# Kernel tuning notes

Hardware: AMD Instinct MI355X
Metric: run time of the kernel (lower is better)

## Reference

```python
import jax, jax.numpy as jnp
import numpy as np

B, V, P, L, D = 8, 16, 128, 16, 128
PD = L * D  # patch_dim = patch_size * d_model = 2048


def _layernorm(x, g, b, eps=1e-5):
    mu = jnp.mean(x, axis=-1, keepdims=True)
    var = jnp.mean(jnp.square(x - mu), axis=-1, keepdims=True)
    return (x - mu) / jnp.sqrt(var + eps) * g + b


def setup_inputs() -> dict:
    key = jax.random.key(0)
    ks = jax.random.split(key, 24)
    x = jax.random.normal(ks[0], (B, V, P, L, D), jnp.float32)
    m = jax.random.randint(ks[1], (B, V, V), 0, 2) > 0
    var_mask = m & ~jnp.eye(V, dtype=bool)[None]  # keep self-attention unmasked

    def lin_w(k, fan_in, fan_out):
        return jax.random.normal(k, (fan_in, fan_out), jnp.float32) * (1.0 / np.sqrt(fan_in))

    inp = {"x": x, "var_mask": var_mask}
    # Attn_PatchLevel (attn1): query / shared kv / out projections
    inp["w_q1"] = lin_w(ks[2], PD, PD); inp["b_q1"] = jnp.zeros((PD,), jnp.float32)
    inp["w_kv1"] = lin_w(ks[3], PD, PD); inp["b_kv1"] = jnp.zeros((PD,), jnp.float32)
    inp["w_o1"] = lin_w(ks[4], PD, PD); inp["b_o1"] = jnp.zeros((PD,), jnp.float32)
    # Attn_VarLevel (attn2)
    inp["w_q2"] = lin_w(ks[5], PD, PD); inp["b_q2"] = jnp.zeros((PD,), jnp.float32)
    inp["w_kv2"] = lin_w(ks[6], PD, PD); inp["b_kv2"] = jnp.zeros((PD,), jnp.float32)
    inp["w_o2"] = lin_w(ks[7], PD, PD); inp["b_o2"] = jnp.zeros((PD,), jnp.float32)
    # LayerNorms
    inp["g1"] = jnp.ones((PD,), jnp.float32); inp["be1"] = jnp.zeros((PD,), jnp.float32)
    inp["g2"] = jnp.ones((PD,), jnp.float32); inp["be2"] = jnp.zeros((PD,), jnp.float32)
    inp["g3"] = jnp.ones((PD,), jnp.float32); inp["be3"] = jnp.zeros((PD,), jnp.float32)
    # FFN
    inp["w_l1"] = lin_w(ks[8], PD, 4 * PD); inp["b_l1"] = jnp.zeros((4 * PD,), jnp.float32)
    inp["w_l2"] = lin_w(ks[9], 4 * PD, PD); inp["b_l2"] = jnp.zeros((PD,), jnp.float32)
    return inp


def reference(x, var_mask,
              w_q1, b_q1, w_kv1, b_kv1, w_o1, b_o1,
              w_q2, b_q2, w_kv2, b_kv2, w_o2, b_o2,
              g1, be1, g2, be2, g3, be3,
              w_l1, b_l1, w_l2, b_l2):
    b, v, p, l, d = x.shape
    pd = l * d
    scale = 1.0 / np.sqrt(pd)
    x = x.reshape(b, v, p, pd)

    # ---- Attn_PatchLevel (mask=None -> no masking; keys and values share kv_projection) ----
    q = x @ w_q1 + b_q1
    kv = x @ w_kv1 + b_kv1  # keys == values in the original module
    scores = jnp.einsum('bvpd,bvsd->bvps', q, kv)  # [B,V,P,P]
    attn = jax.nn.softmax(scale * scores, axis=-1)  # dropout is identity at eval
    a1 = jnp.einsum('bvps,bvsd->bvpd', attn, kv) @ w_o1 + b_o1
    x = _layernorm(x + a1, g1, be1)

    # ---- Attn_VarLevel over variables, per patch ----
    x = x.transpose(0, 2, 1, 3)  # [B,P,V,PD]
    q = x @ w_q2 + b_q2
    kv = x @ w_kv2 + b_kv2
    scores = jnp.einsum('bpvd,bprd->bpvr', q, kv)  # [B,P,V,V]
    scores = jnp.where(var_mask[:, None, :, :], -jnp.inf, scores)
    attn = jax.nn.softmax(scale * scores, axis=-1)
    a2 = jnp.einsum('bpvr,bprd->bpvd', attn, kv) @ w_o2 + b_o2
    x = _layernorm(x + a2, g2, be2)

    # ---- FFN (torch nn.GELU default = exact erf) ----
    z = jax.nn.gelu(x @ w_l1 + b_l1, approximate=False)
    x = x + z @ w_l2 + b_l2

    x_out = _layernorm(x, g3, be3).transpose(0, 2, 1, 3)  # [B,V,P,PD]
    x_next = x_out.reshape(b, v, p // 2, 2 * l, d)
    return x_out, x_next
```

## Files before the change

kernel.cpp:

```cpp
#include <hip/hip_runtime.h>
#include <math.h>


using u16   = unsigned short;
using f32x4 = __attribute__((ext_vector_type(4))) float;
using bf16x8= __attribute__((ext_vector_type(8))) __bf16;
using u16x8 = __attribute__((ext_vector_type(8))) u16;
using u16x4 = __attribute__((ext_vector_type(4))) u16;

#define NROWS 16384
#define PD    2048
#define MEMBAR asm volatile("" ::: "memory")

__device__ __forceinline__ float bf2f(u16 u) {
    unsigned v = ((unsigned)u) << 16;
    return __builtin_bit_cast(float, v);
}
__device__ __forceinline__ u16 f2bf(float f) {
    unsigned u = __builtin_bit_cast(unsigned, f);
    u += 0x7FFFu + ((u >> 16) & 1u);
    return (u16)(u >> 16);
}
__device__ __forceinline__ void gload_lds16(const void* g, void* l) {
    __builtin_amdgcn_global_load_lds((const __attribute__((address_space(1))) void*)g,
                                     (__attribute__((address_space(3))) void*)l, 16, 0, 0);
}
__device__ __forceinline__ void block_barrier() {
    MEMBAR; __builtin_amdgcn_s_barrier(); MEMBAR;
}

template<int GELU>
__global__ __launch_bounds__(512, 2)
void gemm256(const u16* __restrict__ A, int lda,
             const u16* __restrict__ B, int ldb,
             u16* __restrict__ C1, u16* __restrict__ C2, int ncut, int ldc,
             const float* __restrict__ bias1, const float* __restrict__ bias2,
             int K, int NT, int CM, int CN)
{
    __shared__ __align__(16) char smem[131072];

    const int tid  = threadIdx.x;
    const int wv   = tid >> 6;
    const int wm   = wv >> 2;
    const int wn   = wv & 3;
    const int lane = tid & 63;
    const int fr   = lane & 15;
    const int fks16= (lane >> 4) * 16;
    const int rmask= (fr & 7) << 4;
    const int kb0  = fks16 ^ rmask;
    const int kb1  = (64 + fks16) ^ rmask;

    const int xcd = blockIdx.x & 7;
    const int ii  = blockIdx.x >> 3;
    const int RY  = NT / CN;
    const int mt  = (xcd / RY) * CM + (ii / CN);
    const int nt  = (xcd % RY) * CN + (ii % CN);
    const int m0  = mt * 256;
    const int n0  = nt * 256;

    const int rsub = tid >> 3;
    const int cswE = (((tid & 7) * 16) ^ ((rsub & 7) << 4)) >> 1;
    const int waveByte = wv * 1024;

    auto stage = [&](const u16* mat, int ld, int row0, int k0, int regionByte) {
        const u16* g0 = mat + (size_t)(row0 + rsub) * ld + k0 + cswE;
        gload_lds16(g0,                   smem + regionByte + waveByte);
        gload_lds16(g0 + (size_t)ld * 64, smem + regionByte + 8192 + waveByte);
    };

    const int aRowByte = (wm * 128 + fr) * 128;
    const int bRowByte = (wn * 64 + fr) * 128;

    const int KT = K >> 6;

    stage(A, lda, m0,       0, 0);
    stage(B, ldb, n0,       0, 32768);
    stage(A, lda, m0 + 128, 0, 16384);
    stage(B, ldb, n0 + 128, 0, 49152);
    stage(B, ldb, n0,      64, 98304);
    stage(A, lda, m0,      64, 65536);
    asm volatile("s_waitcnt vmcnt(4)" ::: "memory");
    __builtin_amdgcn_s_barrier();

    bf16x8 a[4][2], b0[2][2], b1[2][2];
    f32x4  acc[8][4] = {};

    for (int t = 0; t < KT; ++t) {
        const int Ab = (t & 1) ? 65536 : 0;
        const int Bb = Ab + 32768;
        const int Ob = Ab ^ 65536;
        const bool s1 = (t + 1 < KT), s2 = (t + 2 < KT);

        #pragma unroll
        for (int mi = 0; mi < 4; ++mi) {
            const int rb = Ab + aRowByte + mi * 2048;
            a[mi][0] = *(const bf16x8*)(smem + rb + kb0);
            a[mi][1] = *(const bf16x8*)(smem + rb + kb1);
        }
        #pragma unroll
        for (int nj = 0; nj < 2; ++nj) {
            const int rb = Bb + bRowByte + nj * 2048;
            b0[nj][0] = *(const bf16x8*)(smem + rb + kb0);
            b0[nj][1] = *(const bf16x8*)(smem + rb + kb1);
        }
        if (s1) stage(B, ldb, n0 + 128, (t + 1) << 6, Ob + 49152);
        __builtin_amdgcn_s_barrier();
        asm volatile("s_waitcnt lgkmcnt(0)" ::: "memory");
        __builtin_amdgcn_sched_barrier(0);
        __builtin_amdgcn_s_setprio(1);
        #pragma unroll
        for (int mi = 0; mi < 4; ++mi)
            #pragma unroll
            for (int nj = 0; nj < 2; ++nj) {
                acc[mi][nj] = __builtin_amdgcn_mfma_f32_16x16x32_bf16(a[mi][0], b0[nj][0], acc[mi][nj], 0, 0, 0);
                acc[mi][nj] = __builtin_amdgcn_mfma_f32_16x16x32_bf16(a[mi][1], b0[nj][1], acc[mi][nj], 0, 0, 0);
            }
        __builtin_amdgcn_s_setprio(0);
        __builtin_amdgcn_s_barrier();

        #pragma unroll
        for (int nj = 0; nj < 2; ++nj) {
            const int rb = Bb + bRowByte + 4096 + nj * 2048;
            b1[nj][0] = *(const bf16x8*)(smem + rb + kb0);
            b1[nj][1] = *(const bf16x8*)(smem + rb + kb1);
        }
        if (s1) stage(A, lda, m0 + 128, (t + 1) << 6, Ob + 16384);
        __builtin_amdgcn_s_barrier();
        asm volatile("s_waitcnt lgkmcnt(0)" ::: "memory");
        __builtin_amdgcn_sched_barrier(0);
        __builtin_amdgcn_s_setprio(1);
        #pragma unroll
        for (int mi = 0; mi < 4; ++mi)
            #pragma unroll
            for (int nj = 0; nj < 2; ++nj) {
                acc[mi][2 + nj] = __builtin_amdgcn_mfma_f32_16x16x32_bf16(a[mi][0], b1[nj][0], acc[mi][2 + nj], 0, 0, 0);
                acc[mi][2 + nj] = __builtin_amdgcn_mfma_f32_16x16x32_bf16(a[mi][1], b1[nj][1], acc[mi][2 + nj], 0, 0, 0);
            }
        __builtin_amdgcn_s_setprio(0);
        __builtin_amdgcn_s_barrier();

        #pragma unroll
        for (int mi = 0; mi < 4; ++mi) {
            const int rb = Ab + aRowByte + 8192 + mi * 2048;
            a[mi][0] = *(const bf16x8*)(smem + rb + kb0);
            a[mi][1] = *(const bf16x8*)(smem + rb + kb1);
        }
        if (s2) stage(B, ldb, n0, (t + 2) << 6, Bb);
        __builtin_amdgcn_s_barrier();
        asm volatile("s_waitcnt lgkmcnt(0)" ::: "memory");
        __builtin_amdgcn_sched_barrier(0);
        __builtin_amdgcn_s_setprio(1);
        #pragma unroll
        for (int mi = 0; mi < 4; ++mi)
            #pragma unroll
            for (int nj = 0; nj < 2; ++nj) {
                acc[4 + mi][nj] = __builtin_amdgcn_mfma_f32_16x16x32_bf16(a[mi][0], b0[nj][0], acc[4 + mi][nj], 0, 0, 0);
                acc[4 + mi][nj] = __builtin_amdgcn_mfma_f32_16x16x32_bf16(a[mi][1], b0[nj][1], acc[4 + mi][nj], 0, 0, 0);
            }
        __builtin_amdgcn_s_setprio(0);
        __builtin_amdgcn_s_barrier();

        if (s2) stage(A, lda, m0, (t + 2) << 6, Ab);
        __builtin_amdgcn_s_barrier();
        __builtin_amdgcn_s_setprio(1);
        #pragma unroll
        for (int mi = 0; mi < 4; ++mi)
            #pragma unroll
            for (int nj = 0; nj < 2; ++nj) {
                acc[4 + mi][2 + nj] = __builtin_amdgcn_mfma_f32_16x16x32_bf16(a[mi][0], b1[nj][0], acc[4 + mi][2 + nj], 0, 0, 0);
                acc[4 + mi][2 + nj] = __builtin_amdgcn_mfma_f32_16x16x32_bf16(a[mi][1], b1[nj][1], acc[4 + mi][2 + nj], 0, 0, 0);
            }
        __builtin_amdgcn_s_setprio(0);
        if (s2) { asm volatile("s_waitcnt vmcnt(4)" ::: "memory"); }
        else    { asm volatile("s_waitcnt vmcnt(0)" ::: "memory"); }
        __builtin_amdgcn_s_barrier();
    }

    u16* Cout; const float* bs; int ncol;
    if (n0 < ncut) { Cout = C1; bs = bias1; ncol = n0; }
    else           { Cout = C2; bs = bias2; ncol = n0 - ncut; }

    block_barrier();
    u16* lsu = (u16*)smem;
    const int lcolB = wn * 64 + fr;
    const int lrowB = wm * 128 + (lane >> 4) * 4;
    #pragma unroll
    for (int nj = 0; nj < 4; ++nj) {
        const int lcol = lcolB + nj * 16;
        const float bb = bs[ncol + lcol];
        #pragma unroll
        for (int mi = 0; mi < 8; ++mi) {
            #pragma unroll
            for (int j = 0; j < 4; ++j) {
                float v = acc[mi][nj][j] + bb;
                if constexpr (GELU) v = 0.5f * v * (1.f + erff(v * 0.70710678118f));
                lsu[(lrowB + mi * 16 + j) * 256 + lcol] = f2bf(v);
            }
        }
    }
    block_barrier();
    const int hp = tid & 31;
    const int r0 = tid >> 5;
    #pragma unroll
    for (int ps = 0; ps < 16; ++ps) {
        const int r = ps * 16 + r0;
        u16x8 v = *(const u16x8*)&lsu[r * 256 + hp * 8];
        *(u16x8*)&Cout[(size_t)(m0 + r) * ldc + ncol + hp * 8] = v;
    }
}

template<int OUTF32, int HASBIAS>
__global__ __launch_bounds__(256, 2)
void gemm_nt(const u16* __restrict__ A, long sAg, int lda,
             const u16* __restrict__ B, long sBg, int ldb,
             void* __restrict__ Cv, long sCg, int ldc,
             const float* __restrict__ bias, int K, float scale)
{
    __shared__ __align__(16) u16 lsA[128 * 32];
    __shared__ __align__(16) u16 lsB[128 * 32];

    const int tid  = threadIdx.x;
    const int w    = tid >> 6;
    const int lane = tid & 63;
    const int m0   = blockIdx.x * 128;
    const int n0   = blockIdx.y * 128;
    A += (long)blockIdx.z * sAg;
    B += (long)blockIdx.z * sBg;

    const int wr = w >> 1, wc = w & 1;
    f32x4 acc[4][4] = {};

    const int srow = lane >> 2;
    const int skc  = (lane & 3) * 8;
    const int rA0  = 32 * w + srow;
    const int rA1  = rA0 + 16;
    const size_t aoff0 = (size_t)(m0 + rA0) * lda + skc;
    const size_t aoff1 = (size_t)(m0 + rA1) * lda + skc;
    const size_t boff0 = (size_t)(n0 + rA0) * ldb + skc;
    const size_t boff1 = (size_t)(n0 + rA1) * ldb + skc;
    u16* lA0 = lsA + 1024 * w;
    u16* lA1 = lA0 + 512;
    u16* lB0 = lsB + 1024 * w;
    u16* lB1 = lB0 + 512;

    const int fr = lane & 15;
    const int fk = (lane >> 4) * 8;

    for (int k0 = 0; k0 < K; k0 += 32) {
        gload_lds16(A + aoff0 + k0, lA0);
        gload_lds16(A + aoff1 + k0, lA1);
        gload_lds16(B + boff0 + k0, lB0);
        gload_lds16(B + boff1 + k0, lB1);
        __syncthreads();

        bf16x8 af[4], bf[4];
        #pragma unroll
        for (int m = 0; m < 4; m++)
            af[m] = *(const bf16x8*)&lsA[(wr * 64 + m * 16 + fr) * 32 + fk];
        #pragma unroll
        for (int n = 0; n < 4; n++)
            bf[n] = *(const bf16x8*)&lsB[(wc * 64 + n * 16 + fr) * 32 + fk];
        #pragma unroll
        for (int m = 0; m < 4; m++)
            #pragma unroll
            for (int n = 0; n < 4; n++)
                acc[m][n] = __builtin_amdgcn_mfma_f32_16x16x32_bf16(af[m], bf[n], acc[m][n], 0, 0, 0);
        __syncthreads();
    }

    float* Cf = (float*)Cv;
    u16*   Cb = (u16*)Cv;
    const int crow0 = m0 + wr * 64 + (lane >> 4) * 4;
    const int ccol0 = n0 + wc * 64 + fr;
    const long cbase = (long)blockIdx.z * sCg;
    #pragma unroll
    for (int n = 0; n < 4; n++) {
        const int col = ccol0 + n * 16;
        float bb = 0.f;
        if constexpr (HASBIAS) bb = bias[col];
        #pragma unroll
        for (int m = 0; m < 4; m++) {
            #pragma unroll
            for (int j = 0; j < 4; j++) {
                const int row = crow0 + m * 16 + j;
                float v = acc[m][n][j] + bb;
                const long idx = cbase + (long)row * ldc + col;
                if constexpr (OUTF32) Cf[idx] = v * scale;
                else                  Cb[idx] = f2bf(v);
            }
        }
    }
}

__global__ __launch_bounds__(256)
void wtrans_kernel(const float* __restrict__ in, u16* __restrict__ out, int R, int C)
{
    __shared__ float tile[32][33];
    const int c0 = blockIdx.x * 32, r0 = blockIdx.y * 32;
    const int tx = threadIdx.x & 31, ty = threadIdx.x >> 5;
    #pragma unroll
    for (int i = ty; i < 32; i += 8)
        tile[i][tx] = in[(size_t)(r0 + i) * C + c0 + tx];
    __syncthreads();
    #pragma unroll
    for (int i = ty; i < 32; i += 8)
        out[(size_t)(c0 + i) * R + r0 + tx] = f2bf(tile[tx][i]);
}

__global__ __launch_bounds__(256)
void kvtrans_kernel(const u16* __restrict__ in, u16* __restrict__ out)
{
    __shared__ u16 tile[32][33];
    const int g = blockIdx.z;
    const int n0 = blockIdx.x * 32, m0 = blockIdx.y * 32;
    const int tx = threadIdx.x & 31, ty = threadIdx.x >> 5;
    #pragma unroll
    for (int i = ty; i < 32; i += 8)
        tile[i][tx] = in[(size_t)(g * 128 + m0 + i) * 2048 + n0 + tx];
    __syncthreads();
    #pragma unroll
    for (int i = ty; i < 32; i += 8)
        out[(size_t)g * 262144 + (size_t)(n0 + i) * 128 + m0 + tx] = tile[tx][i];
}

__global__ __launch_bounds__(256)
void cvt_f32_bf16(const float* __restrict__ in, u16* __restrict__ out)
{
    const long i = ((long)blockIdx.x * 256 + threadIdx.x) * 4;
    float4 v = *(const float4*)(in + i);
    u16x4 o;
    o[0] = f2bf(v.x); o[1] = f2bf(v.y); o[2] = f2bf(v.z); o[3] = f2bf(v.w);
    *(u16x4*)(out + i) = o;
}

template<int FINAL>
__global__ __launch_bounds__(256)
void ln_kernel(const float* __restrict__ resid, const u16* __restrict__ add,
               const float* __restrict__ gam, const float* __restrict__ bet,
               u16* __restrict__ xb, float* __restrict__ o1, float* __restrict__ o2)
{
    const long row = blockIdx.x;
    const int  t   = threadIdx.x;
    const long base = row * PD + t * 8;

    u16x8  av = *(const u16x8*)(add + base);
    float4 r0 = *(const float4*)(resid + base);
    float4 r1 = *(const float4*)(resid + base + 4);
    float y[8];
    y[0] = r0.x + bf2f(av[0]); y[1] = r0.y + bf2f(av[1]);
    y[2] = r0.z + bf2f(av[2]); y[3] = r0.w + bf2f(av[3]);
    y[4] = r1.x + bf2f(av[4]); y[5] = r1.y + bf2f(av[5]);
    y[6] = r1.z + bf2f(av[6]); y[7] = r1.w + bf2f(av[7]);

    float s1 = 0.f, s2 = 0.f;
    #pragma unroll
    for (int j = 0; j < 8; j++) { s1 += y[j]; s2 += y[j] * y[j]; }
    #pragma unroll
    for (int d = 1; d < 64; d <<= 1) { s1 += __shfl_xor(s1, d); s2 += __shfl_xor(s2, d); }
    __shared__ float red[8];
    const int w = t >> 6;
    if ((t & 63) == 0) { red[w] = s1; red[4 + w] = s2; }
    __syncthreads();
    s1 = red[0] + red[1] + red[2] + red[3];
    s2 = red[4] + red[5] + red[6] + red[7];
    const float mean = s1 * (1.f / PD);
    const float var  = s2 * (1.f / PD) - mean * mean;
    const float rstd = rsqrtf(var + 1e-5f);

    float4 g0 = *(const float4*)(gam + t * 8);
    float4 g1 = *(const float4*)(gam + t * 8 + 4);
    float4 b0 = *(const float4*)(bet + t * 8);
    float4 b1 = *(const float4*)(bet + t * 8 + 4);
    float gv[8] = {g0.x, g0.y, g0.z, g0.w, g1.x, g1.y, g1.z, g1.w};
    float bv[8] = {b0.x, b0.y, b0.z, b0.w, b1.x, b1.y, b1.z, b1.w};

    float o[8];
    #pragma unroll
    for (int j = 0; j < 8; j++) o[j] = (y[j] - mean) * rstd * gv[j] + bv[j];

    if constexpr (FINAL) {
        float4 p0 = {o[0], o[1], o[2], o[3]}, p1 = {o[4], o[5], o[6], o[7]};
        *(float4*)(o1 + base) = p0; *(float4*)(o1 + base + 4) = p1;
        *(float4*)(o2 + base) = p0; *(float4*)(o2 + base + 4) = p1;
    } else {
        u16x8 ob;
        #pragma unroll
        for (int j = 0; j < 8; j++) ob[j] = f2bf(o[j]);
        *(u16x8*)(xb + base) = ob;
        float4 p0 = {o[0], o[1], o[2], o[3]}, p1 = {o[4], o[5], o[6], o[7]};
        *(float4*)(o1 + base) = p0; *(float4*)(o1 + base + 4) = p1;
    }
}

__global__ __launch_bounds__(256)
void softmax128_kernel(const float* __restrict__ S, u16* __restrict__ P)
{
    const int row  = blockIdx.x * 4 + (threadIdx.x >> 6);
    const int lane = threadIdx.x & 63;
    const float2 v = *(const float2*)(S + (size_t)row * 128 + lane * 2);
    float mx = fmaxf(v.x, v.y);
    #pragma unroll
    for (int d = 1; d < 64; d <<= 1) mx = fmaxf(mx, __shfl_xor(mx, d));
    const float e0 = __expf(v.x - mx), e1 = __expf(v.y - mx);
    float sm = e0 + e1;
    #pragma unroll
    for (int d = 1; d < 64; d <<= 1) sm += __shfl_xor(sm, d);
    const float inv = 1.f / sm;
    unsigned o = (unsigned)f2bf(e0 * inv) | ((unsigned)f2bf(e1 * inv) << 16);
    *(unsigned*)(P + (size_t)row * 128 + lane * 2) = o;
}

__global__ void detect_mask_kernel(const unsigned char* __restrict__ m, int* __restrict__ flag)
{
    __shared__ int s;
    if (threadIdx.x == 0) s = 0;
    __syncthreads();
    int acc = 0;
    for (int i = threadIdx.x; i < 2048; i += 256)
        if (i & 3) acc |= m[i];
    if (acc) atomicOr(&s, 1);
    __syncthreads();
    if (threadIdx.x == 0) *flag = s;
}

__global__ __launch_bounds__(64)
void attn2_kernel(u16* __restrict__ Q, const u16* __restrict__ KV,
                  const void* __restrict__ mask, const int* __restrict__ mflag,
                  float scale)
{
    const int g = blockIdx.x;
    const int b = g >> 7, p = g & 127;
    const int lane = threadIdx.x;

    const size_t groupbase = ((size_t)(b * 16) * 128 + p) * PD;
    const size_t vstride   = (size_t)128 * PD;

    const int am   = lane & 15;
    const int koff = (lane >> 4) * 8;
    const u16* qp = Q  + groupbase + (size_t)am * vstride + koff;
    const u16* kp = KV + groupbase + (size_t)am * vstride + koff;

    f32x4 acc = {0.f, 0.f, 0.f, 0.f};
    for (int k0 = 0; k0 < PD; k0 += 32) {
        bf16x8 a  = *(const bf16x8*)(qp + k0);
        bf16x8 bb = *(const bf16x8*)(kp + k0);
        acc = __builtin_amdgcn_mfma_f32_16x16x32_bf16(a, bb, acc, 0, 0, 0);
    }

    const int vk = lane & 15;
    const int hi = lane >> 4;
    const int mf = *mflag;
    __shared__ float PL[16][16];
    float pv[4];
    #pragma unroll
    for (int j = 0; j < 4; j++) {
        const int vq = hi * 4 + j;
        float s = acc[j] * scale;
        const int midx = b * 256 + vq * 16 + vk;
        int msk;
        if (mf) msk = ((const unsigned char*)mask)[midx];
        else    msk = ((const int*)mask)[midx];
        if (msk) s = -1e30f;
        pv[j] = s;
    }
    #pragma unroll
    for (int j = 0; j < 4; j++) {
        float mx = pv[j];
        #pragma unroll
        for (int d = 1; d < 16; d <<= 1) mx = fmaxf(mx, __shfl_xor(mx, d));
        const float e = __expf(pv[j] - mx);
        float sm = e;
        #pragma unroll
        for (int d = 1; d < 16; d <<= 1) sm += __shfl_xor(sm, d);
        pv[j] = e / sm;
    }
    #pragma unroll
    for (int j = 0; j < 4; j++) PL[hi * 4 + j][vk] = pv[j];
    __syncthreads();

    const u16* kvr[16];
    #pragma unroll
    for (int v = 0; v < 16; v++) kvr[v] = KV + groupbase + (size_t)v * vstride;

    for (int vqt = 0; vqt < 16; vqt += 4) {
        float pr[4][16];
        #pragma unroll
        for (int q = 0; q < 4; q++)
            #pragma unroll
            for (int k = 0; k < 16; k++) pr[q][k] = PL[vqt + q][k];
        u16* o0 = Q + groupbase + (size_t)(vqt + 0) * vstride;
        u16* o1 = Q + groupbase + (size_t)(vqt + 1) * vstride;
        u16* o2 = Q + groupbase + (size_t)(vqt + 2) * vstride;
        u16* o3 = Q + groupbase + (size_t)(vqt + 3) * vstride;
        for (int n0 = 0; n0 < PD; n0 += 64) {
            const int n = n0 + lane;
            float a0 = 0.f, a1 = 0.f, a2 = 0.f, a3 = 0.f;
            #pragma unroll
            for (int k = 0; k < 16; k++) {
                const float kvv = bf2f(kvr[k][n]);
                a0 += pr[0][k] * kvv; a1 += pr[1][k] * kvv;
                a2 += pr[2][k] * kvv; a3 += pr[3][k] * kvv;
            }
            o0[n] = f2bf(a0); o1[n] = f2bf(a1); o2[n] = f2bf(a2); o3[n] = f2bf(a3);
        }
    }
}

extern "C" void kernel_launch(void* const* d_in, const int* in_sizes, int n_in,
                              void* d_out, int out_size, void* d_ws, size_t ws_size,
                              hipStream_t stream)
{
    const float* x0    = (const float*)d_in[0];
    const void*  vmask = d_in[1];
    const float* w_q1  = (const float*)d_in[2];  const float* b_q1  = (const float*)d_in[3];
    const float* w_kv1 = (const float*)d_in[4];  const float* b_kv1 = (const float*)d_in[5];
    const float* w_o1  = (const float*)d_in[6];  const float* b_o1  = (const float*)d_in[7];
    const float* w_q2  = (const float*)d_in[8];  const float* b_q2  = (const float*)d_in[9];
    const float* w_kv2 = (const float*)d_in[10]; const float* b_kv2 = (const float*)d_in[11];
    const float* w_o2  = (const float*)d_in[12]; const float* b_o2  = (const float*)d_in[13];
    const float* g1 = (const float*)d_in[14]; const float* be1 = (const float*)d_in[15];
    const float* g2 = (const float*)d_in[16]; const float* be2 = (const float*)d_in[17];
    const float* g3 = (const float*)d_in[18]; const float* be3 = (const float*)d_in[19];
    const float* w_l1 = (const float*)d_in[20]; const float* b_l1 = (const float*)d_in[21];
    const float* w_l2 = (const float*)d_in[22]; const float* b_l2 = (const float*)d_in[23];

    char* ws = (char*)d_ws;
    size_t off = 0;
    auto alloc = [&](size_t bytes) { size_t o = off; off += (bytes + 255) & ~(size_t)255; return o; };
    const size_t oWQ1  = alloc(8388608),  oWKV1 = alloc(8388608),  oWO1 = alloc(8388608);
    const size_t oWQ2  = alloc(8388608),  oWKV2 = alloc(8388608),  oWO2 = alloc(8388608);
    const size_t oWL1  = alloc(33554432), oWL2  = alloc(33554432);
    const size_t oXB   = alloc(67108864);
    const size_t oQ    = alloc(67108864);
    const size_t oKV   = alloc(67108864);
    const size_t oKVT  = alloc(67108864);
    const size_t oR    = alloc(134217728);
    const size_t oS    = alloc(8388608);
    const size_t oP1   = alloc(4194304);
    const size_t oFLAG = alloc(256);
    if (ws_size < off) return;

    u16* WQ1T = (u16*)(ws + oWQ1);  u16* WKV1T = (u16*)(ws + oWKV1); u16* WO1T = (u16*)(ws + oWO1);
    u16* WQ2T = (u16*)(ws + oWQ2);  u16* WKV2T = (u16*)(ws + oWKV2); u16* WO2T = (u16*)(ws + oWO2);
    u16* WL1T = (u16*)(ws + oWL1);  u16* WL2T  = (u16*)(ws + oWL2);
    u16* XB   = (u16*)(ws + oXB);   u16* Q     = (u16*)(ws + oQ);
    u16* KV   = (u16*)(ws + oKV);   u16* KVT   = (u16*)(ws + oKVT);
    float* R  = (float*)(ws + oR);  float* S   = (float*)(ws + oS);
    u16* P1   = (u16*)(ws + oP1);   int* FLAG  = (int*)(ws + oFLAG);
    u16* H    = Q;
    u16* F    = KVT;

    const float scale = 0.02209708691f;
    float* out0 = (float*)d_out;
    float* out1 = out0 + (size_t)NROWS * PD;

    detect_mask_kernel<<<1, 256, 0, stream>>>((const unsigned char*)vmask, FLAG);

    wtrans_kernel<<<dim3(64, 64), 256, 0, stream>>>(w_q1,  WQ1T,  2048, 2048);
    wtrans_kernel<<<dim3(64, 64), 256, 0, stream>>>(w_kv1, WKV1T, 2048, 2048);
    wtrans_kernel<<<dim3(64, 64), 256, 0, stream>>>(w_o1,  WO1T,  2048, 2048);
    wtrans_kernel<<<dim3(64, 64), 256, 0, stream>>>(w_q2,  WQ2T,  2048, 2048);
    wtrans_kernel<<<dim3(64, 64), 256, 0, stream>>>(w_kv2, WKV2T, 2048, 2048);
    wtrans_kernel<<<dim3(64, 64), 256, 0, stream>>>(w_o2,  WO2T,  2048, 2048);
    wtrans_kernel<<<dim3(256, 64), 256, 0, stream>>>(w_l1, WL1T, 2048, 8192);
    wtrans_kernel<<<dim3(64, 256), 256, 0, stream>>>(w_l2, WL2T, 8192, 2048);

    cvt_f32_bf16<<<32768, 256, 0, stream>>>(x0, XB);

    const int BIG = 1 << 30;

    gemm256<0><<<1024, 512, 0, stream>>>(XB, 2048, WQ1T, 2048, Q, KV, 2048, 2048,
                                         b_q1, b_kv1, 2048, 16, 32, 4);
    kvtrans_kernel<<<dim3(64, 4, 128), 256, 0, stream>>>(KV, KVT);
    gemm_nt<1,0><<<dim3(1,1,128), 256, 0, stream>>>(Q, 262144, 2048, KV, 262144, 2048, S, 16384, 128, nullptr, 2048, scale);
    softmax128_kernel<<<4096, 256, 0, stream>>>(S, P1);
    gemm_nt<0,0><<<dim3(1,16,128), 256, 0, stream>>>(P1, 16384, 128, KVT, 262144, 128, Q, 262144, 2048, nullptr, 128, 1.f);
    gemm256<0><<<512, 512, 0, stream>>>(Q, 2048, WO1T, 2048, KV, KV, BIG, 2048,
                                        b_o1, b_o1, 2048, 8, 32, 2);
    ln_kernel<0><<<NROWS, 256, 0, stream>>>(x0, KV, g1, be1, XB, R, nullptr);

    gemm256<0><<<1024, 512, 0, stream>>>(XB, 2048, WQ2T, 2048, Q, KV, 2048, 2048,
                                         b_q2, b_kv2, 2048, 16, 32, 4);
    attn2_kernel<<<1024, 64, 0, stream>>>(Q, KV, vmask, FLAG, scale);
    gemm256<0><<<512, 512, 0, stream>>>(Q, 2048, WO2T, 2048, KV, KV, BIG, 2048,
                                        b_o2, b_o2, 2048, 8, 32, 2);
    ln_kernel<0><<<NROWS, 256, 0, stream>>>(R, KV, g2, be2, XB, R, nullptr);

    for (int c = 0; c < 2; c++) {
        const size_t rows = (size_t)c * 8192;
        gemm256<1><<<1024, 512, 0, stream>>>(XB + rows * 2048, 2048, WL1T, 2048,
                                             H, H, BIG, 8192, b_l1, b_l1, 2048, 32, 32, 4);
        gemm256<0><<<256, 512, 0, stream>>>(H, 8192, WL2T, 8192,
                                            F + rows * 2048, F + rows * 2048, BIG, 2048,
                                            b_l2, b_l2, 8192, 8, 32, 1);
    }
    ln_kernel<1><<<NROWS, 256, 0, stream>>>(R, F, g3, be3, nullptr, out0, out1);
}
```

Measured before the change: 2.474 ms.

## Fuse patch-attention scores with softmax and keep residual stream in bf16

Replaces the separate scores GEMM plus softmax kernel with one kernel per group. It computes the 128x128 QK^T tile in LDS and applies softmax there, so the fp32 score matrix never goes through global memory. It also drops the fp32 residual buffer R: the later layernorms read the bf16 XB copy as the residual instead of reloading fp32, which cuts memory traffic. In exchange the residual path loses precision, and the fused kernel runs only 128 blocks with a single-stage load loop.

```diff
diff --git a/kernel.cpp b/kernel.cpp
--- a/kernel.cpp
+++ b/kernel.cpp
@@ -292,6 +292,85 @@
     }
 }
 
+__global__ __launch_bounds__(256, 1)
+void scores_softmax_kernel(const u16* __restrict__ Q, const u16* __restrict__ KVp,
+                           u16* __restrict__ P, float scale)
+{
+    __shared__ __align__(16) u16 lsA[128 * 32];
+    __shared__ __align__(16) u16 lsB[128 * 32];
+    __shared__ float SL[128][130];
+
+    const int g = blockIdx.x;
+    const u16* A = Q   + (size_t)g * 262144;
+    const u16* B = KVp + (size_t)g * 262144;
+
+    const int tid  = threadIdx.x;
+    const int w    = tid >> 6;
+    const int lane = tid & 63;
+    const int wr = w >> 1, wc = w & 1;
+    f32x4 acc[4][4] = {};
+
+    const int srow = lane >> 2;
+    const int skc  = (lane & 3) * 8;
+    const int rA0  = 32 * w + srow;
+    const int rA1  = rA0 + 16;
+    const size_t aoff0 = (size_t)rA0 * 2048 + skc;
+    const size_t aoff1 = (size_t)rA1 * 2048 + skc;
+    u16* lA0 = lsA + 1024 * w;
+    u16* lA1 = lA0 + 512;
+    u16* lB0 = lsB + 1024 * w;
+    u16* lB1 = lB0 + 512;
+
+    const int fr = lane & 15;
+    const int fk = (lane >> 4) * 8;
+
+    for (int k0 = 0; k0 < 2048; k0 += 32) {
+        gload_lds16(A + aoff0 + k0, lA0);
+        gload_lds16(A + aoff1 + k0, lA1);
+        gload_lds16(B + aoff0 + k0, lB0);
+        gload_lds16(B + aoff1 + k0, lB1);
+        __syncthreads();
+        bf16x8 af[4], bf[4];
+        #pragma unroll
+        for (int m = 0; m < 4; m++)
+            af[m] = *(const bf16x8*)&lsA[(wr * 64 + m * 16 + fr) * 32 + fk];
+        #pragma unroll
+        for (int n = 0; n < 4; n++)
+            bf[n] = *(const bf16x8*)&lsB[(wc * 64 + n * 16 + fr) * 32 + fk];
+        #pragma unroll
+        for (int m = 0; m < 4; m++)
+            #pragma unroll
+            for (int n = 0; n < 4; n++)
+                acc[m][n] = __builtin_amdgcn_mfma_f32_16x16x32_bf16(af[m], bf[n], acc[m][n], 0, 0, 0);
+        __syncthreads();
+    }
+
+    const int crow0 = wr * 64 + (lane >> 4) * 4;
+    const int ccol0 = wc * 64 + fr;
+    #pragma unroll
+    for (int n = 0; n < 4; n++)
+        #pragma unroll
+        for (int m = 0; m < 4; m++)
+            #pragma unroll
+            for (int j = 0; j < 4; j++)
+                SL[crow0 + m * 16 + j][ccol0 + n * 16] = acc[m][n][j] * scale;
+    __syncthreads();
+
+    unsigned* Pout = (unsigned*)(P + (size_t)g * 16384);
+    for (int r = w * 32; r < w * 32 + 32; ++r) {
+        const float v0 = SL[r][lane * 2], v1 = SL[r][lane * 2 + 1];
+        float mx = fmaxf(v0, v1);
+        #pragma unroll
+        for (int d = 1; d < 64; d <<= 1) mx = fmaxf(mx, __shfl_xor(mx, d));
+        const float e0 = __expf(v0 - mx), e1 = __expf(v1 - mx);
+        float sm = e0 + e1;
+        #pragma unroll
+        for (int d = 1; d < 64; d <<= 1) sm += __shfl_xor(sm, d);
+        const float inv = 1.f / sm;
+        Pout[r * 64 + lane] = (unsigned)f2bf(e0 * inv) | ((unsigned)f2bf(e1 * inv) << 16);
+    }
+}
+
 __global__ __launch_bounds__(256)
 void wtrans_kernel(const float* __restrict__ in, u16* __restrict__ out, int R, int C)
 {
@@ -333,9 +412,9 @@
     *(u16x4*)(out + i) = o;
 }
 
-template<int FINAL>
+template<int FINAL, int RESF32>
 __global__ __launch_bounds__(256)
-void ln_kernel(const float* __restrict__ resid, const u16* __restrict__ add,
+void ln_kernel(const void* __restrict__ residv, const u16* __restrict__ add,
                const float* __restrict__ gam, const float* __restrict__ bet,
                u16* __restrict__ xb, float* __restrict__ o1, float* __restrict__ o2)
 {
@@ -343,14 +422,22 @@
     const int  t   = threadIdx.x;
     const long base = row * PD + t * 8;
 
-    u16x8  av = *(const u16x8*)(add + base);
-    float4 r0 = *(const float4*)(resid + base);
-    float4 r1 = *(const float4*)(resid + base + 4);
+    u16x8 av = *(const u16x8*)(add + base);
     float y[8];
-    y[0] = r0.x + bf2f(av[0]); y[1] = r0.y + bf2f(av[1]);
-    y[2] = r0.z + bf2f(av[2]); y[3] = r0.w + bf2f(av[3]);
-    y[4] = r1.x + bf2f(av[4]); y[5] = r1.y + bf2f(av[5]);
-    y[6] = r1.z + bf2f(av[6]); y[7] = r1.w + bf2f(av[7]);
+    if constexpr (RESF32) {
+        const float* resid = (const float*)residv;
+        float4 r0 = *(const float4*)(resid + base);
+        float4 r1 = *(const float4*)(resid + base + 4);
+        y[0] = r0.x + bf2f(av[0]); y[1] = r0.y + bf2f(av[1]);
+        y[2] = r0.z + bf2f(av[2]); y[3] = r0.w + bf2f(av[3]);
+        y[4] = r1.x + bf2f(av[4]); y[5] = r1.y + bf2f(av[5]);
+        y[6] = r1.z + bf2f(av[6]); y[7] = r1.w + bf2f(av[7]);
+    } else {
+        const u16* resid = (const u16*)residv;
+        u16x8 rv = *(const u16x8*)(resid + base);
+        #pragma unroll
+        for (int j = 0; j < 8; j++) y[j] = bf2f(rv[j]) + bf2f(av[j]);
+    }
 
     float s1 = 0.f, s2 = 0.f;
     #pragma unroll
@@ -387,27 +474,7 @@
         #pragma unroll
         for (int j = 0; j < 8; j++) ob[j] = f2bf(o[j]);
         *(u16x8*)(xb + base) = ob;
-        float4 p0 = {o[0], o[1], o[2], o[3]}, p1 = {o[4], o[5], o[6], o[7]};
-        *(float4*)(o1 + base) = p0; *(float4*)(o1 + base + 4) = p1;
-    }
-}
-
-__global__ __launch_bounds__(256)
-void softmax128_kernel(const float* __restrict__ S, u16* __restrict__ P)
-{
-    const int row  = blockIdx.x * 4 + (threadIdx.x >> 6);
-    const int lane = threadIdx.x & 63;
-    const float2 v = *(const float2*)(S + (size_t)row * 128 + lane * 2);
-    float mx = fmaxf(v.x, v.y);
-    #pragma unroll
-    for (int d = 1; d < 64; d <<= 1) mx = fmaxf(mx, __shfl_xor(mx, d));
-    const float e0 = __expf(v.x - mx), e1 = __expf(v.y - mx);
-    float sm = e0 + e1;
-    #pragma unroll
-    for (int d = 1; d < 64; d <<= 1) sm += __shfl_xor(sm, d);
-    const float inv = 1.f / sm;
-    unsigned o = (unsigned)f2bf(e0 * inv) | ((unsigned)f2bf(e1 * inv) << 16);
-    *(unsigned*)(P + (size_t)row * 128 + lane * 2) = o;
+    }
 }
 
 __global__ void detect_mask_kernel(const unsigned char* __restrict__ m, int* __restrict__ flag)
@@ -534,8 +601,6 @@
     const size_t oQ    = alloc(67108864);
     const size_t oKV   = alloc(67108864);
     const size_t oKVT  = alloc(67108864);
-    const size_t oR    = alloc(134217728);
-    const size_t oS    = alloc(8388608);
     const size_t oP1   = alloc(4194304);
     const size_t oFLAG = alloc(256);
     if (ws_size < off) return;
@@ -545,7 +610,6 @@
     u16* WL1T = (u16*)(ws + oWL1);  u16* WL2T  = (u16*)(ws + oWL2);
     u16* XB   = (u16*)(ws + oXB);   u16* Q     = (u16*)(ws + oQ);
     u16* KV   = (u16*)(ws + oKV);   u16* KVT   = (u16*)(ws + oKVT);
-    float* R  = (float*)(ws + oR);  float* S   = (float*)(ws + oS);
     u16* P1   = (u16*)(ws + oP1);   int* FLAG  = (int*)(ws + oFLAG);
     u16* H    = Q;
     u16* F    = KVT;
@@ -572,19 +636,18 @@
     gemm256<0><<<1024, 512, 0, stream>>>(XB, 2048, WQ1T, 2048, Q, KV, 2048, 2048,
                                          b_q1, b_kv1, 2048, 16, 32, 4);
     kvtrans_kernel<<<dim3(64, 4, 128), 256, 0, stream>>>(KV, KVT);
-    gemm_nt<1,0><<<dim3(1,1,128), 256, 0, stream>>>(Q, 262144, 2048, KV, 262144, 2048, S, 16384, 128, nullptr, 2048, scale);
-    softmax128_kernel<<<4096, 256, 0, stream>>>(S, P1);
+    scores_softmax_kernel<<<128, 256, 0, stream>>>(Q, KV, P1, scale);
     gemm_nt<0,0><<<dim3(1,16,128), 256, 0, stream>>>(P1, 16384, 128, KVT, 262144, 128, Q, 262144, 2048, nullptr, 128, 1.f);
     gemm256<0><<<512, 512, 0, stream>>>(Q, 2048, WO1T, 2048, KV, KV, BIG, 2048,
                                         b_o1, b_o1, 2048, 8, 32, 2);
-    ln_kernel<0><<<NROWS, 256, 0, stream>>>(x0, KV, g1, be1, XB, R, nullptr);
+    ln_kernel<0,1><<<NROWS, 256, 0, stream>>>(x0, KV, g1, be1, XB, nullptr, nullptr);
 
     gemm256<0><<<1024, 512, 0, stream>>>(XB, 2048, WQ2T, 2048, Q, KV, 2048, 2048,
                                          b_q2, b_kv2, 2048, 16, 32, 4);
     attn2_kernel<<<1024, 64, 0, stream>>>(Q, KV, vmask, FLAG, scale);
     gemm256<0><<<512, 512, 0, stream>>>(Q, 2048, WO2T, 2048, KV, KV, BIG, 2048,
                                         b_o2, b_o2, 2048, 8, 32, 2);
-    ln_kernel<0><<<NROWS, 256, 0, stream>>>(R, KV, g2, be2, XB, R, nullptr);
+    ln_kernel<0,0><<<NROWS, 256, 0, stream>>>(XB, KV, g2, be2, XB, nullptr, nullptr);
 
     for (int c = 0; c < 2; c++) {
         const size_t rows = (size_t)c * 8192;
@@ -594,5 +657,5 @@
                                             F + rows * 2048, F + rows * 2048, BIG, 2048,
                                             b_l2, b_l2, 8192, 8, 32, 1);
     }
-    ln_kernel<1><<<NROWS, 256, 0, stream>>>(R, F, g3, be3, nullptr, out0, out1);
-}
+    ln_kernel<1,0><<<NROWS, 256, 0, stream>>>(XB, F, g3, be3, nullptr, out0, out1);
+}
```

Result: faster. 2.410 ms (-2.6%).
